# Kernel optimization log

Hardware: AMD Instinct MI355X
Metric: run time of the kernel (lower is better)

Reference implementation:

```python
import jax, jax.numpy as jnp
import numpy as np

DIM = 2048
N_HEADS = 16
Q_RANK = 1536
KV_RANK = 512
D_NOPE = 128
D_ROPE = 64
D_V = 128
EPS = 1e-6
B, S = 2, 2048
ROPE_THETA = 10000.0


def rmsnorm(x, w, eps=EPS):
    return x * jax.lax.rsqrt(jnp.mean(x * x, axis=-1, keepdims=True) + eps) * w


def apply_rope(x):
    # x: [b, h, s, d] with d even; LLaMA-style interleaved pair rotation
    b, h, s, d = x.shape
    inv_freq = 1.0 / (ROPE_THETA ** (jnp.arange(0, d, 2, dtype=jnp.float32) / d))
    ang = jnp.arange(s, dtype=jnp.float32)[:, None] * inv_freq[None, :]  # [s, d/2]
    cos, sin = jnp.cos(ang), jnp.sin(ang)
    xr = x.reshape(b, h, s, d // 2, 2)
    x1, x2 = xr[..., 0], xr[..., 1]
    o1 = x1 * cos - x2 * sin
    o2 = x1 * sin + x2 * cos
    return jnp.stack([o1, o2], axis=-1).reshape(b, h, s, d)


def setup_inputs() -> dict:
    key = jax.random.key(0)
    ks = jax.random.split(key, 10)
    std = 0.02
    return {
        "x": jax.random.normal(ks[0], (B, S, DIM), dtype=jnp.float32),
        "wq_down": jax.random.normal(ks[1], (Q_RANK, DIM), dtype=jnp.float32) * std,
        "q_norm_w": jnp.ones((Q_RANK,), dtype=jnp.float32),
        "wq_up": jax.random.normal(ks[2], (N_HEADS * D_NOPE, Q_RANK), dtype=jnp.float32) * std,
        "wq_rope": jax.random.normal(ks[3], (N_HEADS * D_ROPE, Q_RANK), dtype=jnp.float32) * std,
        "wkv_down": jax.random.normal(ks[4], (KV_RANK, DIM), dtype=jnp.float32) * std,
        "kv_norm_w": jnp.ones((KV_RANK,), dtype=jnp.float32),
        "wkv_up": jax.random.normal(ks[5], (N_HEADS * (D_NOPE + D_V), KV_RANK), dtype=jnp.float32) * std,
        "wk_rope": jax.random.normal(ks[6], (D_ROPE, DIM), dtype=jnp.float32) * std,
        "wo": jax.random.normal(ks[7], (DIM, N_HEADS * D_V), dtype=jnp.float32) * std,
    }


def reference(x, wq_down, q_norm_w, wq_up, wq_rope, wkv_down, kv_norm_w, wkv_up, wk_rope, wo):
    bs, s, _ = x.shape
    # low-rank Q path
    q_c = rmsnorm(x @ wq_down.T, q_norm_w)                              # [b,s,qr]
    q_nope = (q_c @ wq_up.T).reshape(bs, s, N_HEADS, D_NOPE).transpose(0, 2, 1, 3)
    q_pe = (q_c @ wq_rope.T).reshape(bs, s, N_HEADS, D_ROPE).transpose(0, 2, 1, 3)
    # low-rank KV path
    kv_c = rmsnorm(x @ wkv_down.T, kv_norm_w)                           # [b,s,kvr]
    kv_up = (kv_c @ wkv_up.T).reshape(bs, s, N_HEADS, D_NOPE + D_V)
    k_nope = kv_up[..., :D_NOPE].transpose(0, 2, 1, 3)                  # [b,h,s,dn]
    v = kv_up[..., D_NOPE:].transpose(0, 2, 1, 3)                       # [b,h,s,dv]
    # shared rope key (1 head), broadcast across heads
    k_rope = (x @ wk_rope.T).reshape(bs, s, 1, D_ROPE).transpose(0, 2, 1, 3)  # [b,1,s,dr]
    q_pe = apply_rope(q_pe)
    k_rope = apply_rope(k_rope)
    q = jnp.concatenate([q_nope, q_pe], axis=-1)                        # [b,h,s,dn+dr]
    k = jnp.concatenate([k_nope, jnp.broadcast_to(k_rope, (bs, N_HEADS, s, D_ROPE))], axis=-1)
    scale = 1.0 / np.sqrt(D_NOPE + D_ROPE)
    scores = jnp.einsum('bhqd,bhkd->bhqk', q, k) * scale                # [b,h,s,s]
    causal = jnp.tril(jnp.ones((s, s), dtype=bool))
    scores = jnp.where(causal, scores, -jnp.inf)
    probs = jax.nn.softmax(scores, axis=-1)
    out = jnp.einsum('bhqk,bhkv->bhqv', probs, v)                       # [b,h,s,dv]
    out = out.transpose(0, 2, 1, 3).reshape(bs, s, N_HEADS * D_V)
    return out @ wo.T
```

## Files before the change

kernel.cpp:

```cpp
#include <hip/hip_runtime.h>
#include <stdint.h>

typedef _Float16 f16x8 __attribute__((ext_vector_type(8)));
typedef _Float16 f16x4 __attribute__((ext_vector_type(4)));
typedef float fx4 __attribute__((ext_vector_type(4)));

static constexpr int S_LEN = 2048;
static constexpr int BATCH = 2;
static constexpr int TOKENS = BATCH * S_LEN;
static constexpr int DIM = 2048;
static constexpr int NH = 16;
static constexpr int QR = 1536;
static constexpr int KVR = 512;
static constexpr int DN = 128;
static constexpr int DR = 64;
static constexpr int DV = 128;

__device__ __forceinline__ void async16(const _Float16* g, _Float16* lds_base_uniform) {
  __builtin_amdgcn_global_load_lds(
      (const __attribute__((address_space(1))) void*)g,
      (__attribute__((address_space(3))) void*)lds_base_uniform, 16, 0, 0);
}

__device__ __forceinline__ void bar() {
  asm volatile("" ::: "memory");
  __builtin_amdgcn_s_barrier();
  asm volatile("" ::: "memory");
}
#define VMWAIT(n) asm volatile("s_waitcnt vmcnt(" #n ")" ::: "memory")

#define ROR16(x, ctrl) \
  __uint_as_float(__builtin_amdgcn_update_dpp(__float_as_uint(x), __float_as_uint(x), \
                                              (ctrl), 0xF, 0xF, false))

__device__ __forceinline__ void sincos_rev(float ang, float* sn, float* cs) {
  float rev = ang * 0.15915494309189535f;
  rev -= floorf(rev);
  *sn = __builtin_amdgcn_sinf(rev);
  *cs = __builtin_amdgcn_cosf(rev);
}

struct CvtSegs {
  const float* src[9];
  _Float16* dst[9];
  const float* nw[9];
  int nmod[9];
  int n4[9];
  int cum[10];
};
__global__ __launch_bounds__(256) void cvt_all(CvtSegs s) {
  const int b = blockIdx.x;
  int seg = 0;
#pragma unroll
  for (int k = 0; k < 8; ++k) seg += (b >= s.cum[seg + 1]) ? 1 : 0;
  const int i = (b - s.cum[seg]) * 256 + threadIdx.x;
  if (i >= s.n4[seg]) return;
  if (!s.src[seg]) {
    f16x4 z;
    z[0] = (_Float16)0.f; z[1] = (_Float16)0.f;
    z[2] = (_Float16)0.f; z[3] = (_Float16)0.f;
    *(f16x4*)(s.dst[seg] + (size_t)i * 4) = z;
    return;
  }
  fx4 v = *(const fx4*)(s.src[seg] + (size_t)i * 4);
  if (s.nw[seg]) {
    const int c0 = (int)(((size_t)i * 4) % (size_t)s.nmod[seg]);
    fx4 wv = *(const fx4*)(s.nw[seg] + c0);
    v[0] *= wv[0]; v[1] *= wv[1]; v[2] *= wv[2]; v[3] *= wv[3];
  }
  f16x4 o;
  o[0] = (_Float16)v[0]; o[1] = (_Float16)v[1];
  o[2] = (_Float16)v[2]; o[3] = (_Float16)v[3];
  *(f16x4*)(s.dst[seg] + (size_t)i * 4) = o;
}

__global__ __launch_bounds__(512, 1) void gemm_down(
    const _Float16* __restrict__ A,
    const _Float16* __restrict__ W,
    _Float16* __restrict__ qc, _Float16* __restrict__ kvc,
    _Float16* __restrict__ kr,
    float* __restrict__ sums_q, float* __restrict__ sums_kv) {
  __shared__ __attribute__((aligned(16))) _Float16 As[2][128 * 64];
  __shared__ __attribute__((aligned(16))) _Float16 Ws[2][256 * 64];

  const int tid = threadIdx.x;
  const int lane = tid & 63;
  const int wave = tid >> 6;
  const int wrow = wave >> 2;
  const int wcol = wave & 3;
  const int m16 = lane & 15;
  const int quad = lane >> 4;
  const int m0 = blockIdx.y * 128;
  const int n0 = blockIdx.x * 256;
  const int K = DIM;

  auto stageA = [&](int buf, int k0) {
#pragma unroll
    for (int k = 0; k < 2; ++k) {
      const int cb = (wave * 2 + k) * 64;
      const int ch = cb + lane;
      const int r = ch >> 3;
      const int gc = (ch & 7) ^ (r & 7);
      async16(A + (size_t)(m0 + r) * K + k0 + gc * 8, &As[buf][cb * 8]);
    }
  };
  auto stageW = [&](int buf, int k0, int h) {
#pragma unroll
    for (int k = 0; k < 2; ++k) {
      const int cb = (wave * 2 + k) * 64;
      const int ch = cb + lane;
      const int r = ch >> 3;
      const int gc = (ch & 7) ^ (r & 7);
      async16(W + (size_t)(n0 + h * 128 + r) * K + k0 + gc * 8,
              &Ws[buf][(h * 1024 + cb) * 8]);
    }
  };

  const fx4 fz = {0.f, 0.f, 0.f, 0.f};
  fx4 acc[4][4];
#pragma unroll
  for (int i = 0; i < 4; ++i)
#pragma unroll
    for (int j = 0; j < 4; ++j) acc[i][j] = fz;

  f16x8 af[4][2], wf0[2][2], wf1[2][2];

  auto rdA = [&](const _Float16* as) {
#pragma unroll
    for (int mg = 0; mg < 4; ++mg)
#pragma unroll
      for (int ks = 0; ks < 2; ++ks) {
        const int row = mg * 32 + wrow * 16 + m16;
        af[mg][ks] = *(const f16x8*)(&as[(row * 8 + ((ks * 4 + quad) ^ (m16 & 7))) * 8]);
      }
  };
  auto rdB = [&](const _Float16* ws, int nh, f16x8 wf[2][2]) {
#pragma unroll
    for (int ng = 0; ng < 2; ++ng)
#pragma unroll
      for (int ks = 0; ks < 2; ++ks) {
        const int row = nh * 128 + ng * 64 + wcol * 16 + m16;
        wf[ng][ks] = *(const f16x8*)(&ws[(row * 8 + ((ks * 4 + quad) ^ (m16 & 7))) * 8]);
      }
  };
  auto halfMFMA = [&](int nh, f16x8 wf[2][2]) {
    __builtin_amdgcn_s_setprio(1);
#pragma unroll
    for (int ks = 0; ks < 2; ++ks)
#pragma unroll
      for (int mg = 0; mg < 4; ++mg)
#pragma unroll
        for (int ng = 0; ng < 2; ++ng)
          acc[mg][nh * 2 + ng] = __builtin_amdgcn_mfma_f32_16x16x32_f16(
              af[mg][ks], wf[ng][ks], acc[mg][nh * 2 + ng], 0, 0, 0);
    __builtin_amdgcn_s_setprio(0);
  };

  const int nkt = K >> 6;
  stageA(0, 0);
  stageW(0, 0, 0);
  stageW(0, 0, 1);

  for (int t = 0; t < nkt; ++t) {
    const int cur = t & 1;
    const int nb = cur ^ 1;
    const int k0n = (t + 1) * 64;
    const bool more = (t + 1 < nkt);
    const _Float16* as = As[cur];
    const _Float16* ws = Ws[cur];

    VMWAIT(2);
    bar();
    rdA(as);
    rdB(ws, 0, wf0);
    if (more) stageA(nb, k0n);
    halfMFMA(0, wf0);

    if (more) { VMWAIT(2); } else { VMWAIT(0); }
    bar();
    rdB(ws, 1, wf1);
    if (more) { stageW(nb, k0n, 0); stageW(nb, k0n, 1); }
    halfMFMA(1, wf1);
  }

  const int bx = blockIdx.x;
  if (bx < 8) {
#pragma unroll
    for (int ng = 0; ng < 4; ++ng) {
      const int col = n0 + ng * 64 + wcol * 16 + m16;
#pragma unroll
      for (int mg = 0; mg < 4; ++mg)
#pragma unroll
        for (int r = 0; r < 4; ++r) {
          const size_t row = (size_t)(m0 + mg * 32 + wrow * 16 + quad * 4 + r);
          const _Float16 v = (_Float16)acc[mg][ng][r];
          if (bx < 6) qc[row * 1536 + col] = v;
          else        kvc[row * 512 + col - 1536] = v;
        }
    }
    float* sums = (bx < 6) ? sums_q : sums_kv;
#pragma unroll
    for (int mg = 0; mg < 4; ++mg)
#pragma unroll
      for (int r = 0; r < 4; ++r) {
        float p = 0.f;
#pragma unroll
        for (int ng = 0; ng < 4; ++ng) p += acc[mg][ng][r] * acc[mg][ng][r];
        p += __shfl_xor(p, 1);
        p += __shfl_xor(p, 2);
        p += __shfl_xor(p, 4);
        p += __shfl_xor(p, 8);
        if (m16 == 0)
          atomicAdd(&sums[m0 + mg * 32 + wrow * 16 + quad * 4 + r], p);
      }
  } else {
#pragma unroll
    for (int ng = 0; ng < 4; ++ng) {
      const int col = n0 + ng * 64 + wcol * 16 + m16;
      if (col < 2112) {
        const int d = col - 2048;
        const int pidx = d >> 1;
        const bool odd = (d & 1);
        const float fr = exp2f(-(float)pidx * 0.4152410118609203f);
#pragma unroll
        for (int mg = 0; mg < 4; ++mg)
#pragma unroll
          for (int r = 0; r < 4; ++r) {
            const size_t row = (size_t)(m0 + mg * 32 + wrow * 16 + quad * 4 + r);
            const int spos = (int)(row & (S_LEN - 1));
            float sn, cs;
            sincos_rev((float)spos * fr, &sn, &cs);
            const float own = acc[mg][ng][r];
            const float oth = __shfl_xor(own, 1);
            const float res = odd ? (oth * sn + own * cs) : (own * cs - oth * sn);
            kr[row * 64 + d] = (_Float16)res;
          }
      } else {
#pragma unroll
        for (int mg = 0; mg < 4; ++mg)
#pragma unroll
          for (int r = 0; r < 4; ++r) (void)__shfl_xor(acc[mg][ng][r], 1);
      }
    }
  }
}

__global__ __launch_bounds__(512, 2) void gemm256_up(
    const _Float16* __restrict__ qc, const _Float16* __restrict__ wqu,
    const _Float16* __restrict__ kvc, const _Float16* __restrict__ wkvu,
    const float* __restrict__ sums_q, const float* __restrict__ sums_kv,
    _Float16* __restrict__ qnope, _Float16* __restrict__ qpe,
    _Float16* __restrict__ knope, _Float16* __restrict__ vT) {
  __shared__ __attribute__((aligned(16))) _Float16 As[2][256 * 64];
  __shared__ __attribute__((aligned(16))) _Float16 Ws[2][256 * 64];

  const int tid = threadIdx.x;
  const int lane = tid & 63;
  const int wave = tid >> 6;
  const int wrow = wave >> 2;
  const int wcol = wave & 3;
  const int m16 = lane & 15;
  const int quad = lane >> 4;
  const int m0 = blockIdx.y * 256;

  const bool isq = ((int)blockIdx.x < 12);
  const int n0 = (isq ? blockIdx.x : blockIdx.x - 12) * 256;
  const _Float16* A = isq ? qc : kvc;
  const _Float16* W = isq ? wqu : wkvu;
  const int K = isq ? QR : KVR;

  auto stageHalf = [&](int buf, int k0, int tensor, int h) {
#pragma unroll
    for (int k = 0; k < 2; ++k) {
      const int cb = (wave * 2 + k) * 64;
      const int ch = cb + lane;
      const int r = ch >> 3;
      const int gc = (ch & 7) ^ (r & 7);
      const int grow = h * 128 + r;
      if (tensor == 0)
        async16(A + (size_t)(m0 + grow) * K + k0 + gc * 8,
                &As[buf][(h * 1024 + cb) * 8]);
      else
        async16(W + (size_t)(n0 + grow) * K + k0 + gc * 8,
                &Ws[buf][(h * 1024 + cb) * 8]);
    }
  };

  const fx4 fz = {0.f, 0.f, 0.f, 0.f};
  fx4 acc[8][4];
#pragma unroll
  for (int i = 0; i < 8; ++i)
#pragma unroll
    for (int j = 0; j < 4; ++j) acc[i][j] = fz;

  f16x8 af[4][2], wf0[2][2], wf1[2][2];

  auto rdA = [&](const _Float16* as, int mh) {
#pragma unroll
    for (int mg = 0; mg < 4; ++mg)
#pragma unroll
      for (int ks = 0; ks < 2; ++ks) {
        const int row = mh * 128 + mg * 32 + wrow * 16 + m16;
        af[mg][ks] = *(const f16x8*)(&as[(row * 8 + ((ks * 4 + quad) ^ (m16 & 7))) * 8]);
      }
  };
  auto rdB = [&](const _Float16* ws, int nh, f16x8 wf[2][2]) {
#pragma unroll
    for (int ng = 0; ng < 2; ++ng)
#pragma unroll
      for (int ks = 0; ks < 2; ++ks) {
        const int row = nh * 128 + ng * 64 + wcol * 16 + m16;
        wf[ng][ks] = *(const f16x8*)(&ws[(row * 8 + ((ks * 4 + quad) ^ (m16 & 7))) * 8]);
      }
  };
  auto quadMFMA = [&](int mh, int nh, f16x8 wf[2][2]) {
    __builtin_amdgcn_s_setprio(1);
#pragma unroll
    for (int ks = 0; ks < 2; ++ks)
#pragma unroll
      for (int mg = 0; mg < 4; ++mg)
#pragma unroll
        for (int ng = 0; ng < 2; ++ng)
          acc[mh * 4 + mg][nh * 2 + ng] = __builtin_amdgcn_mfma_f32_16x16x32_f16(
              af[mg][ks], wf[ng][ks], acc[mh * 4 + mg][nh * 2 + ng], 0, 0, 0);
    __builtin_amdgcn_s_setprio(0);
  };

  const int nkt = K >> 6;
  stageHalf(0, 0, 0, 0);
  stageHalf(0, 0, 1, 0);
  stageHalf(0, 0, 1, 1);
  stageHalf(0, 0, 0, 1);

  for (int t = 0; t < nkt; ++t) {
    const int cur = t & 1;
    const int nb = cur ^ 1;
    const int k0n = (t + 1) * 64;
    const bool more = (t + 1 < nkt);
    const _Float16* as = As[cur];
    const _Float16* ws = Ws[cur];

    VMWAIT(4);
    bar();
    rdA(as, 0);
    rdB(ws, 0, wf0);
    if (more) stageHalf(nb, k0n, 0, 0);
    quadMFMA(0, 0, wf0);

    if (more) { VMWAIT(4); } else { VMWAIT(2); }
    bar();
    rdB(ws, 1, wf1);
    if (more) stageHalf(nb, k0n, 1, 0);
    quadMFMA(0, 1, wf1);

    if (more) { VMWAIT(4); } else { VMWAIT(0); }
    bar();
    rdA(as, 1);
    if (more) stageHalf(nb, k0n, 1, 1);
    quadMFMA(1, 1, wf1);

    bar();
    if (more) stageHalf(nb, k0n, 0, 1);
    quadMFMA(1, 0, wf0);
  }

  const float* rs = isq ? sums_q : sums_kv;
  const float invNC = isq ? (1.0f / (float)QR) : (1.0f / (float)KVR);
  float rsq[8][4];
#pragma unroll
  for (int mg = 0; mg < 8; ++mg)
#pragma unroll
    for (int r = 0; r < 4; ++r)
      rsq[mg][r] = rsqrtf(rs[m0 + mg * 32 + wrow * 16 + quad * 4 + r] * invNC + 1e-6f);

#pragma unroll
  for (int ng = 0; ng < 4; ++ng) {
    const int col = n0 + ng * 64 + wcol * 16 + m16;
    if (isq) {
#pragma unroll
      for (int mg = 0; mg < 8; ++mg)
#pragma unroll
        for (int r = 0; r < 4; ++r) {
          const size_t row = (size_t)(m0 + mg * 32 + wrow * 16 + quad * 4 + r);
          const _Float16 v = (_Float16)(acc[mg][ng][r] * rsq[mg][r]);
          if (col < 2048) qnope[row * 2048 + col] = v;
          else qpe[row * 1024 + col - 2048] = v;
        }
    } else {
      const int head = col >> 8;
      const int sub = col & 255;
      if (sub < 128) {
#pragma unroll
        for (int mg = 0; mg < 8; ++mg)
#pragma unroll
          for (int r = 0; r < 4; ++r) {
            const size_t row = (size_t)(m0 + mg * 32 + wrow * 16 + quad * 4 + r);
            knope[row * 2048 + head * 128 + sub] =
                (_Float16)(acc[mg][ng][r] * rsq[mg][r]);
          }
      } else {
        const int dv = sub - 128;
#pragma unroll
        for (int mg = 0; mg < 8; ++mg) {
          f16x4 v;
#pragma unroll
          for (int r = 0; r < 4; ++r) v[r] = (_Float16)(acc[mg][ng][r] * rsq[mg][r]);
          *(f16x4*)(&vT[(size_t)(head * 128 + dv) * TOKENS + m0 +
                        mg * 32 + wrow * 16 + quad * 4]) = v;
        }
      }
    }
  }
}

__global__ __launch_bounds__(512, 1) void gemm_out(
    const _Float16* __restrict__ A,
    const _Float16* __restrict__ W,
    float* __restrict__ C) {
  __shared__ __attribute__((aligned(16))) _Float16 As[2][128 * 64];
  __shared__ __attribute__((aligned(16))) _Float16 Ws[2][256 * 64];

  const int tid = threadIdx.x;
  const int lane = tid & 63;
  const int wave = tid >> 6;
  const int wrow = wave >> 2;
  const int wcol = wave & 3;
  const int m16 = lane & 15;
  const int quad = lane >> 4;
  const int m0 = blockIdx.y * 128;
  const int n0 = blockIdx.x * 256;
  const int K = NH * DV;

  auto stageA = [&](int buf, int k0) {
#pragma unroll
    for (int k = 0; k < 2; ++k) {
      const int cb = (wave * 2 + k) * 64;
      const int ch = cb + lane;
      const int r = ch >> 3;
      const int gc = (ch & 7) ^ (r & 7);
      async16(A + (size_t)(m0 + r) * K + k0 + gc * 8, &As[buf][cb * 8]);
    }
  };
  auto stageW = [&](int buf, int k0, int h) {
#pragma unroll
    for (int k = 0; k < 2; ++k) {
      const int cb = (wave * 2 + k) * 64;
      const int ch = cb + lane;
      const int r = ch >> 3;
      const int gc = (ch & 7) ^ (r & 7);
      async16(W + (size_t)(n0 + h * 128 + r) * K + k0 + gc * 8,
              &Ws[buf][(h * 1024 + cb) * 8]);
    }
  };

  const fx4 fz = {0.f, 0.f, 0.f, 0.f};
  fx4 acc[4][4];
#pragma unroll
  for (int i = 0; i < 4; ++i)
#pragma unroll
    for (int j = 0; j < 4; ++j) acc[i][j] = fz;

  f16x8 af[4][2], wf0[2][2], wf1[2][2];

  auto rdA = [&](const _Float16* as) {
#pragma unroll
    for (int mg = 0; mg < 4; ++mg)
#pragma unroll
      for (int ks = 0; ks < 2; ++ks) {
        const int row = mg * 32 + wrow * 16 + m16;
        af[mg][ks] = *(const f16x8*)(&as[(row * 8 + ((ks * 4 + quad) ^ (m16 & 7))) * 8]);
      }
  };
  auto rdB = [&](const _Float16* ws, int nh, f16x8 wf[2][2]) {
#pragma unroll
    for (int ng = 0; ng < 2; ++ng)
#pragma unroll
      for (int ks = 0; ks < 2; ++ks) {
        const int row = nh * 128 + ng * 64 + wcol * 16 + m16;
        wf[ng][ks] = *(const f16x8*)(&ws[(row * 8 + ((ks * 4 + quad) ^ (m16 & 7))) * 8]);
      }
  };
  auto halfMFMA = [&](int nh, f16x8 wf[2][2]) {
    __builtin_amdgcn_s_setprio(1);
#pragma unroll
    for (int ks = 0; ks < 2; ++ks)
#pragma unroll
      for (int mg = 0; mg < 4; ++mg)
#pragma unroll
        for (int ng = 0; ng < 2; ++ng)
          acc[mg][nh * 2 + ng] = __builtin_amdgcn_mfma_f32_16x16x32_f16(
              af[mg][ks], wf[ng][ks], acc[mg][nh * 2 + ng], 0, 0, 0);
    __builtin_amdgcn_s_setprio(0);
  };

  const int nkt = K >> 6;
  stageA(0, 0);
  stageW(0, 0, 0);
  stageW(0, 0, 1);

  for (int t = 0; t < nkt; ++t) {
    const int cur = t & 1;
    const int nb = cur ^ 1;
    const int k0n = (t + 1) * 64;
    const bool more = (t + 1 < nkt);
    const _Float16* as = As[cur];
    const _Float16* ws = Ws[cur];

    VMWAIT(2);
    bar();
    rdA(as);
    rdB(ws, 0, wf0);
    if (more) stageA(nb, k0n);
    halfMFMA(0, wf0);

    if (more) { VMWAIT(2); } else { VMWAIT(0); }
    bar();
    rdB(ws, 1, wf1);
    if (more) { stageW(nb, k0n, 0); stageW(nb, k0n, 1); }
    halfMFMA(1, wf1);
  }

#pragma unroll
  for (int ng = 0; ng < 4; ++ng) {
    const int col = n0 + ng * 64 + wcol * 16 + m16;
#pragma unroll
    for (int mg = 0; mg < 4; ++mg)
#pragma unroll
      for (int r = 0; r < 4; ++r) {
        const size_t row = (size_t)(m0 + mg * 32 + wrow * 16 + quad * 4 + r);
        C[row * 2048 + col] = acc[mg][ng][r];
      }
  }
}

__global__ __launch_bounds__(512, 2) void mla_attn(
    const _Float16* __restrict__ qn,
    const _Float16* __restrict__ qp,
    const _Float16* __restrict__ kn,
    const _Float16* __restrict__ kr,
    const _Float16* __restrict__ vT,
    _Float16* __restrict__ out)
{
  __shared__ __attribute__((aligned(16))) _Float16 Ks[2][768 * 8];
  __shared__ __attribute__((aligned(16))) _Float16 Vs[2][512 * 8];
  __shared__ __attribute__((aligned(16))) _Float16 Ps[8][16][40];

  const int bid = blockIdx.x;
  const int j = bid >> 5;
  const int bh = bid & 31;
  const int b = bh >> 4;
  const int h = bh & 15;
  const int q16 = 15 - j;
  const int qb = q16 * 128;
  const int tok0 = b * S_LEN;

  const int tid = threadIdx.x;
  const int lane = tid & 63;
  const int wave = tid >> 6;
  const int m16 = lane & 15;
  const int quad = lane >> 4;
  const int R0 = qb + wave * 16;

  auto stageKV = [&](int buf, int kbase) {
#pragma unroll
    for (int jj = 0; jj < 3; ++jj) {
      const int idx = wave * 3 + jj;
      if (idx < 12) {
        const int ch = idx * 2 + (lane >> 5);
        const int key = lane & 31;
        const _Float16* g = (ch < 16)
            ? kn + (size_t)(tok0 + kbase + key) * 2048 + h * 128 + ch * 8
            : kr + (size_t)(tok0 + kbase + key) * 64 + (ch - 16) * 8;
        async16(g, &Ks[buf][idx * 512]);
      } else if (idx < 20) {
        const int iv = idx - 12;
        const int p = iv * 64 + lane;
        const int L = p ^ ((p >> 3) & 3);
        const int dv = L >> 2;
        const int qcc = L & 3;
        async16(vT + (size_t)(h * 128 + dv) * TOKENS + tok0 + kbase + qcc * 8,
                &Vs[buf][iv * 512]);
      }
    }
  };

  const float scale2 = 0.07216878364870323f * 1.4426950408889634f;
  const fx4 fz = {0.f, 0.f, 0.f, 0.f};

  f16x8 qf[6];
  {
    const int srow = qb + wave * 16 + m16;
    const size_t t = (size_t)(tok0 + srow);
#pragma unroll
    for (int kk = 0; kk < 4; ++kk)
      qf[kk] = *(const f16x8*)(qn + t * 2048 + h * 128 + kk * 32 + quad * 8);
#pragma unroll
    for (int kk = 0; kk < 2; ++kk) {
      f16x8 v = *(const f16x8*)(qp + t * 1024 + h * 64 + kk * 32 + quad * 8);
      f16x8 o;
      const int i0 = kk * 16 + quad * 4;
#pragma unroll
      for (int jj = 0; jj < 4; ++jj) {
        const float ang = (float)srow * exp2f(-(float)(i0 + jj) * 0.4152410118609203f);
        float sn, cs;
        sincos_rev(ang, &sn, &cs);
        const float x1 = (float)v[2 * jj], x2 = (float)v[2 * jj + 1];
        o[2 * jj]     = (_Float16)(x1 * cs - x2 * sn);
        o[2 * jj + 1] = (_Float16)(x1 * sn + x2 * cs);
      }
      qf[4 + kk] = o;
    }
  }

  fx4 oacc[9];
#pragma unroll
  for (int n = 0; n < 9; ++n) oacc[n] = fz;
  float mst[4];
#pragma unroll
  for (int r = 0; r < 4; ++r) mst[r] = -3.0e38f;
  f16x8 vones;
#pragma unroll
  for (int e = 0; e < 8; ++e) vones[e] = (_Float16)1.0f;

  const int nkt = (qb >> 5) + 4;

  stageKV(0, 0);
  for (int kt = 0; kt < nkt; ++kt) {
    const int kbase = kt * 32;
    __syncthreads();
    if (kt + 1 < nkt) stageKV((kt + 1) & 1, kbase + 32);

    const bool live = (kbase <= R0 + 15);
    if (!live) continue;
    const _Float16* ks = Ks[kt & 1];
    const _Float16* vs = Vs[kt & 1];

    fx4 sc[2];
    sc[0] = fz; sc[1] = fz;
    __builtin_amdgcn_s_setprio(1);
#pragma unroll
    for (int kk = 0; kk < 6; ++kk) {
#pragma unroll
      for (int n = 0; n < 2; ++n) {
        f16x8 kf = *(const f16x8*)(&ks[(kk * 128 + quad * 32 + n * 16 + m16) * 8]);
        sc[n] = __builtin_amdgcn_mfma_f32_16x16x32_f16(qf[kk], kf, sc[n], 0, 0, 0);
      }
    }
    __builtin_amdgcn_s_setprio(0);

    f16x8 vf[8];
#pragma unroll
    for (int n8 = 0; n8 < 8; ++n8) {
      const int c0 = (n8 * 16 + m16) * 4 + quad;
      vf[n8] = *(const f16x8*)(&vs[(c0 ^ ((c0 >> 3) & 3)) * 8]);
    }

    const bool needmask = (kbase + 31 > R0);
    float alpha[4];
    bool any_upd = false;
#pragma unroll
    for (int r = 0; r < 4; ++r) {
      float v0 = sc[0][r] * scale2;
      float v1 = sc[1][r] * scale2;
      if (needmask) {
        const int qrow = R0 + quad * 4 + r;
        if (kbase + m16 > qrow)      v0 = -3.0e38f;
        if (kbase + 16 + m16 > qrow) v1 = -3.0e38f;
      }
      const float pre = fmaxf(v0, v1);
      float al = 1.0f;
      if (__any(pre > mst[r] + 10.0f)) {
        float mx = pre;
        mx = fmaxf(mx, ROR16(mx, 0x128));
        mx = fmaxf(mx, ROR16(mx, 0x124));
        mx = fmaxf(mx, ROR16(mx, 0x122));
        mx = fmaxf(mx, ROR16(mx, 0x121));
        const float mn = fmaxf(mst[r], mx);
        al = exp2f(mst[r] - mn);
        mst[r] = mn;
        any_upd = true;
      }
      alpha[r] = al;
      const float p0 = exp2f(v0 - mst[r]);
      const float p1 = exp2f(v1 - mst[r]);
      _Float16* pr = &Ps[wave][quad * 4 + r][0];
      pr[m16] = (_Float16)p0;
      pr[16 + m16] = (_Float16)p1;
    }
    if (any_upd) {
#pragma unroll
      for (int n8 = 0; n8 < 9; ++n8)
#pragma unroll
        for (int r = 0; r < 4; ++r) oacc[n8][r] *= alpha[r];
    }

    f16x8 pf = *(const f16x8*)(&Ps[wave][m16][quad * 8]);
    __builtin_amdgcn_s_setprio(1);
#pragma unroll
    for (int n8 = 0; n8 < 8; ++n8)
      oacc[n8] = __builtin_amdgcn_mfma_f32_16x16x32_f16(pf, vf[n8], oacc[n8], 0, 0, 0);
    oacc[8] = __builtin_amdgcn_mfma_f32_16x16x32_f16(pf, vones, oacc[8], 0, 0, 0);
    __builtin_amdgcn_s_setprio(0);
  }

  float inv[4];
#pragma unroll
  for (int r = 0; r < 4; ++r) inv[r] = 1.0f / oacc[8][r];
#pragma unroll
  for (int n8 = 0; n8 < 8; ++n8) {
#pragma unroll
    for (int r = 0; r < 4; ++r) {
      const size_t t = (size_t)(tok0 + qb + wave * 16 + quad * 4 + r);
      out[t * 2048 + h * 128 + n8 * 16 + m16] = (_Float16)(oacc[n8][r] * inv[r]);
    }
  }
}

extern "C" void kernel_launch(void* const* d_in, const int* in_sizes, int n_in,
                              void* d_out, int out_size, void* d_ws, size_t ws_size,
                              hipStream_t stream) {
  const float* x         = (const float*)d_in[0];
  const float* wq_down   = (const float*)d_in[1];
  const float* q_norm_w  = (const float*)d_in[2];
  const float* wq_up     = (const float*)d_in[3];
  const float* wq_rope   = (const float*)d_in[4];
  const float* wkv_down  = (const float*)d_in[5];
  const float* kv_norm_w = (const float*)d_in[6];
  const float* wkv_up    = (const float*)d_in[7];
  const float* wk_rope   = (const float*)d_in[8];
  const float* wo        = (const float*)d_in[9];
  float* out = (float*)d_out;

  char* ws = (char*)d_ws;
  size_t off = 0;
  auto alloc = [&](size_t bytes) {
    char* p = ws + off;
    off += (bytes + 255) & ~(size_t)255;
    return p;
  };
  _Float16* x_h     = (_Float16*)alloc((size_t)TOKENS * DIM * 2);
  _Float16* wA_h    = (_Float16*)alloc((size_t)2304 * DIM * 2);
  _Float16* wquqr_h = (_Float16*)alloc((size_t)3072 * QR * 2);
  _Float16* wkvu_h  = (_Float16*)alloc((size_t)NH * 256 * KVR * 2);
  _Float16* wo_h    = (_Float16*)alloc((size_t)DIM * NH * DV * 2);
  _Float16* qc_h    = (_Float16*)alloc((size_t)TOKENS * QR * 2);
  _Float16* kvc_h   = (_Float16*)alloc((size_t)TOKENS * KVR * 2);
  _Float16* qnope_h = (_Float16*)alloc((size_t)TOKENS * 2048 * 2);
  _Float16* qpe_h   = (_Float16*)alloc((size_t)TOKENS * 1024 * 2);
  _Float16* knope_h = (_Float16*)alloc((size_t)TOKENS * 2048 * 2);
  _Float16* vT_h    = (_Float16*)alloc((size_t)2048 * TOKENS * 2);
  _Float16* krope_h = (_Float16*)alloc((size_t)TOKENS * DR * 2);
  _Float16* attn_h  = (_Float16*)alloc((size_t)TOKENS * 2048 * 2);
  float* sq_h       = (float*)alloc((size_t)TOKENS * 4);
  float* skv_h      = (float*)alloc((size_t)TOKENS * 4);

  CvtSegs cs;
  const float* srcs[9] = {x, wq_down, wq_up, wq_rope, wkv_down, wk_rope, wkv_up, wo,
                          nullptr};
  _Float16* dsts[9] = {x_h, wA_h, wquqr_h, wquqr_h + (size_t)2048 * QR,
                       wA_h + (size_t)1536 * DIM, wA_h + (size_t)2048 * DIM,
                       wkvu_h, wo_h, (_Float16*)sq_h};
  const float* nws[9] = {nullptr, nullptr, q_norm_w, q_norm_w, nullptr, nullptr,
                         kv_norm_w, nullptr, nullptr};
  const int nmods[9] = {4, 4, QR, QR, 4, 4, KVR, 4, 4};
  const size_t ns[9] = {(size_t)TOKENS * DIM, (size_t)QR * DIM, (size_t)2048 * QR,
                        (size_t)1024 * QR, (size_t)KVR * DIM, (size_t)DR * DIM,
                        (size_t)NH * 256 * KVR, (size_t)DIM * NH * DV,
                        (size_t)2 * TOKENS * 2};
  int cum = 0;
  for (int i = 0; i < 9; ++i) {
    cs.src[i] = srcs[i];
    cs.dst[i] = dsts[i];
    cs.nw[i] = nws[i];
    cs.nmod[i] = nmods[i];
    cs.n4[i] = (int)(ns[i] / 4);
    cs.cum[i] = cum;
    cum += (cs.n4[i] + 255) / 256;
  }
  cs.cum[9] = cum;
  cvt_all<<<dim3(cum), 256, 0, stream>>>(cs);

  gemm_down<<<dim3(9, 32), 512, 0, stream>>>(x_h, wA_h, qc_h, kvc_h, krope_h,
                                             sq_h, skv_h);
  gemm256_up<<<dim3(12 + 16, TOKENS / 256), 512, 0, stream>>>(
      qc_h, wquqr_h, kvc_h, wkvu_h, sq_h, skv_h,
      qnope_h, qpe_h, knope_h, vT_h);
  mla_attn<<<dim3(512), 512, 0, stream>>>(qnope_h, qpe_h, knope_h, krope_h, vT_h, attn_h);
  gemm_out<<<dim3(8, 32), 512, 0, stream>>>(attn_h, wo_h, out);
}
```

Measured before the change: 454.8 us.

## Retile down-projection GEMM to 128x128 tiles with triple-buffered K=32 stages

Replaces the 128x256-tile, 512-thread down-projection GEMM with 128x128 tiles, 256 threads and a three-stage K=32 async load pipeline. The grid grows from 9x32 to 17x32 blocks, so the last column block wastes less work on padding (2176 instead of 2304 weight rows). The intent is better load balance across CUs, more blocks in flight and deeper prefetch. In exchange each tile reuses loaded data less and there are more barriers per unit of K.

```diff
diff --git a/kernel.cpp b/kernel.cpp
--- a/kernel.cpp
+++ b/kernel.cpp
@@ -74,45 +74,36 @@
   *(f16x4*)(s.dst[seg] + (size_t)i * 4) = o;
 }
 
-__global__ __launch_bounds__(512, 1) void gemm_down(
-    const _Float16* __restrict__ A,
-    const _Float16* __restrict__ W,
-    _Float16* __restrict__ qc, _Float16* __restrict__ kvc,
-    _Float16* __restrict__ kr,
-    float* __restrict__ sums_q, float* __restrict__ sums_kv) {
-  __shared__ __attribute__((aligned(16))) _Float16 As[2][128 * 64];
-  __shared__ __attribute__((aligned(16))) _Float16 Ws[2][256 * 64];
-
+__global__ __launch_bounds__(256) void gemm_down(const _Float16* __restrict__ A,
+                                                 const _Float16* __restrict__ W,
+                                                 _Float16* __restrict__ qc,
+                                                 _Float16* __restrict__ kvc,
+                                                 _Float16* __restrict__ kr,
+                                                 float* __restrict__ sums_q,
+                                                 float* __restrict__ sums_kv) {
+  __shared__ __attribute__((aligned(16))) _Float16 As[3][128 * 32];
+  __shared__ __attribute__((aligned(16))) _Float16 Ws[3][128 * 32];
   const int tid = threadIdx.x;
   const int lane = tid & 63;
   const int wave = tid >> 6;
-  const int wrow = wave >> 2;
-  const int wcol = wave & 3;
+  const int wr = (wave >> 1) * 64;
+  const int wc = (wave & 1) * 64;
   const int m16 = lane & 15;
   const int quad = lane >> 4;
+  const int swz = (m16 >> 1) & 3;
   const int m0 = blockIdx.y * 128;
-  const int n0 = blockIdx.x * 256;
+  const int n0 = blockIdx.x * 128;
   const int K = DIM;
 
-  auto stageA = [&](int buf, int k0) {
-#pragma unroll
-    for (int k = 0; k < 2; ++k) {
-      const int cb = (wave * 2 + k) * 64;
+  auto stage = [&](int buf, int k0) {
+#pragma unroll
+    for (int p = 0; p < 2; ++p) {
+      const int cb = p * 256 + wave * 64;
       const int ch = cb + lane;
-      const int r = ch >> 3;
-      const int gc = (ch & 7) ^ (r & 7);
-      async16(A + (size_t)(m0 + r) * K + k0 + gc * 8, &As[buf][cb * 8]);
-    }
-  };
-  auto stageW = [&](int buf, int k0, int h) {
-#pragma unroll
-    for (int k = 0; k < 2; ++k) {
-      const int cb = (wave * 2 + k) * 64;
-      const int ch = cb + lane;
-      const int r = ch >> 3;
-      const int gc = (ch & 7) ^ (r & 7);
-      async16(W + (size_t)(n0 + h * 128 + r) * K + k0 + gc * 8,
-              &Ws[buf][(h * 1024 + cb) * 8]);
+      const int r = ch >> 2;
+      const int c8 = ((ch & 3) ^ ((r >> 1) & 3)) * 8;
+      async16(A + (size_t)(m0 + r) * K + k0 + c8, &As[buf][cb * 8]);
+      async16(W + (size_t)(n0 + r) * K + k0 + c8, &Ws[buf][cb * 8]);
     }
   };
 
@@ -123,125 +114,84 @@
 #pragma unroll
     for (int j = 0; j < 4; ++j) acc[i][j] = fz;
 
-  f16x8 af[4][2], wf0[2][2], wf1[2][2];
-
-  auto rdA = [&](const _Float16* as) {
-#pragma unroll
-    for (int mg = 0; mg < 4; ++mg)
-#pragma unroll
-      for (int ks = 0; ks < 2; ++ks) {
-        const int row = mg * 32 + wrow * 16 + m16;
-        af[mg][ks] = *(const f16x8*)(&as[(row * 8 + ((ks * 4 + quad) ^ (m16 & 7))) * 8]);
-      }
-  };
-  auto rdB = [&](const _Float16* ws, int nh, f16x8 wf[2][2]) {
-#pragma unroll
-    for (int ng = 0; ng < 2; ++ng)
-#pragma unroll
-      for (int ks = 0; ks < 2; ++ks) {
-        const int row = nh * 128 + ng * 64 + wcol * 16 + m16;
-        wf[ng][ks] = *(const f16x8*)(&ws[(row * 8 + ((ks * 4 + quad) ^ (m16 & 7))) * 8]);
-      }
-  };
-  auto halfMFMA = [&](int nh, f16x8 wf[2][2]) {
-    __builtin_amdgcn_s_setprio(1);
-#pragma unroll
-    for (int ks = 0; ks < 2; ++ks)
-#pragma unroll
-      for (int mg = 0; mg < 4; ++mg)
-#pragma unroll
-        for (int ng = 0; ng < 2; ++ng)
-          acc[mg][nh * 2 + ng] = __builtin_amdgcn_mfma_f32_16x16x32_f16(
-              af[mg][ks], wf[ng][ks], acc[mg][nh * 2 + ng], 0, 0, 0);
-    __builtin_amdgcn_s_setprio(0);
-  };
-
-  const int nkt = K >> 6;
-  stageA(0, 0);
-  stageW(0, 0, 0);
-  stageW(0, 0, 1);
-
-  for (int t = 0; t < nkt; ++t) {
-    const int cur = t & 1;
-    const int nb = cur ^ 1;
-    const int k0n = (t + 1) * 64;
-    const bool more = (t + 1 < nkt);
+  const int nkt = K >> 5;
+  stage(0, 0);
+  stage(1, 32);
+  int cur = 0;
+  for (int kt = 0; kt < nkt; ++kt) {
+    if (kt + 1 < nkt) { VMWAIT(4); } else { VMWAIT(0); }
+    bar();
+    if (kt + 2 < nkt) {
+      int b2 = cur + 2; if (b2 >= 3) b2 -= 3;
+      stage(b2, (kt + 2) * 32);
+    }
     const _Float16* as = As[cur];
     const _Float16* ws = Ws[cur];
-
-    VMWAIT(2);
-    bar();
-    rdA(as);
-    rdB(ws, 0, wf0);
-    if (more) stageA(nb, k0n);
-    halfMFMA(0, wf0);
-
-    if (more) { VMWAIT(2); } else { VMWAIT(0); }
-    bar();
-    rdB(ws, 1, wf1);
-    if (more) { stageW(nb, k0n, 0); stageW(nb, k0n, 1); }
-    halfMFMA(1, wf1);
-  }
-
-  const int bx = blockIdx.x;
-  if (bx < 8) {
-#pragma unroll
-    for (int ng = 0; ng < 4; ++ng) {
-      const int col = n0 + ng * 64 + wcol * 16 + m16;
-#pragma unroll
-      for (int mg = 0; mg < 4; ++mg)
+    f16x8 af[4], wf[4];
+#pragma unroll
+    for (int i = 0; i < 4; ++i)
+      af[i] = *(const f16x8*)(&as[((wr + i * 16 + m16) * 4 + (quad ^ swz)) * 8]);
+#pragma unroll
+    for (int j = 0; j < 4; ++j)
+      wf[j] = *(const f16x8*)(&ws[((wc + j * 16 + m16) * 4 + (quad ^ swz)) * 8]);
+#pragma unroll
+    for (int i = 0; i < 4; ++i)
+#pragma unroll
+      for (int j = 0; j < 4; ++j)
+        acc[i][j] = __builtin_amdgcn_mfma_f32_16x16x32_f16(af[i], wf[j], acc[i][j], 0, 0, 0);
+    if (++cur == 3) cur = 0;
+  }
+
+#pragma unroll
+  for (int j = 0; j < 4; ++j) {
+    const int col = n0 + wc + j * 16 + m16;
+    if (col < 2048) {
+#pragma unroll
+      for (int i = 0; i < 4; ++i)
 #pragma unroll
         for (int r = 0; r < 4; ++r) {
-          const size_t row = (size_t)(m0 + mg * 32 + wrow * 16 + quad * 4 + r);
-          const _Float16 v = (_Float16)acc[mg][ng][r];
-          if (bx < 6) qc[row * 1536 + col] = v;
-          else        kvc[row * 512 + col - 1536] = v;
+          const size_t row = (size_t)(m0 + wr + i * 16 + quad * 4 + r);
+          const _Float16 v = (_Float16)acc[i][j][r];
+          if (col < 1536) qc[row * 1536 + col] = v;
+          else            kvc[row * 512 + col - 1536] = v;
         }
-    }
-    float* sums = (bx < 6) ? sums_q : sums_kv;
-#pragma unroll
-    for (int mg = 0; mg < 4; ++mg)
+    } else if (col < 2112) {
+      const int d = col - 2048;
+      const int pidx = d >> 1;
+      const bool odd = (d & 1);
+      const float fr = exp2f(-(float)pidx * 0.4152410118609203f);
+#pragma unroll
+      for (int i = 0; i < 4; ++i)
+#pragma unroll
+        for (int r = 0; r < 4; ++r) {
+          const size_t row = (size_t)(m0 + wr + i * 16 + quad * 4 + r);
+          const int spos = (int)(row & (S_LEN - 1));
+          float sn, cs;
+          sincos_rev((float)spos * fr, &sn, &cs);
+          const float own = acc[i][j][r];
+          const float oth = __shfl_xor(own, 1);
+          const float res = odd ? (oth * sn + own * cs) : (own * cs - oth * sn);
+          kr[row * 64 + d] = (_Float16)res;
+        }
+    }
+  }
+
+  if (n0 < 2048) {
+    float* sums = (n0 < 1536) ? sums_q : sums_kv;
+#pragma unroll
+    for (int i = 0; i < 4; ++i)
 #pragma unroll
       for (int r = 0; r < 4; ++r) {
         float p = 0.f;
 #pragma unroll
-        for (int ng = 0; ng < 4; ++ng) p += acc[mg][ng][r] * acc[mg][ng][r];
+        for (int j = 0; j < 4; ++j) p += acc[i][j][r] * acc[i][j][r];
         p += __shfl_xor(p, 1);
         p += __shfl_xor(p, 2);
         p += __shfl_xor(p, 4);
         p += __shfl_xor(p, 8);
         if (m16 == 0)
-          atomicAdd(&sums[m0 + mg * 32 + wrow * 16 + quad * 4 + r], p);
-      }
-  } else {
-#pragma unroll
-    for (int ng = 0; ng < 4; ++ng) {
-      const int col = n0 + ng * 64 + wcol * 16 + m16;
-      if (col < 2112) {
-        const int d = col - 2048;
-        const int pidx = d >> 1;
-        const bool odd = (d & 1);
-        const float fr = exp2f(-(float)pidx * 0.4152410118609203f);
-#pragma unroll
-        for (int mg = 0; mg < 4; ++mg)
-#pragma unroll
-          for (int r = 0; r < 4; ++r) {
-            const size_t row = (size_t)(m0 + mg * 32 + wrow * 16 + quad * 4 + r);
-            const int spos = (int)(row & (S_LEN - 1));
-            float sn, cs;
-            sincos_rev((float)spos * fr, &sn, &cs);
-            const float own = acc[mg][ng][r];
-            const float oth = __shfl_xor(own, 1);
-            const float res = odd ? (oth * sn + own * cs) : (own * cs - oth * sn);
-            kr[row * 64 + d] = (_Float16)res;
-          }
-      } else {
-#pragma unroll
-        for (int mg = 0; mg < 4; ++mg)
-#pragma unroll
-          for (int r = 0; r < 4; ++r) (void)__shfl_xor(acc[mg][ng][r], 1);
-      }
-    }
+          atomicAdd(&sums[m0 + wr + i * 16 + quad * 4 + r], p);
+      }
   }
 }
 
@@ -739,7 +689,7 @@
     return p;
   };
   _Float16* x_h     = (_Float16*)alloc((size_t)TOKENS * DIM * 2);
-  _Float16* wA_h    = (_Float16*)alloc((size_t)2304 * DIM * 2);
+  _Float16* wA_h    = (_Float16*)alloc((size_t)2176 * DIM * 2);
   _Float16* wquqr_h = (_Float16*)alloc((size_t)3072 * QR * 2);
   _Float16* wkvu_h  = (_Float16*)alloc((size_t)NH * 256 * KVR * 2);
   _Float16* wo_h    = (_Float16*)alloc((size_t)DIM * NH * DV * 2);
@@ -780,8 +730,10 @@
   cs.cum[9] = cum;
   cvt_all<<<dim3(cum), 256, 0, stream>>>(cs);
 
-  gemm_down<<<dim3(9, 32), 512, 0, stream>>>(x_h, wA_h, qc_h, kvc_h, krope_h,
-                                             sq_h, skv_h);
+  const unsigned gm = TOKENS / 128;
+
+  gemm_down<<<dim3(17, gm), 256, 0, stream>>>(x_h, wA_h, qc_h, kvc_h, krope_h,
+                                              sq_h, skv_h);
   gemm256_up<<<dim3(12 + 16, TOKENS / 256), 512, 0, stream>>>(
       qc_h, wquqr_h, kvc_h, wkvu_h, sq_h, skv_h,
       qnope_h, qpe_h, knope_h, vT_h);
```

Result: faster. 445.0 us (-2.1%).
